# Kernel optimization log

Measured on AMD Instinct MI355X. Metric: run time of the kernel, lower is better.

Reference implementation:

```python
import math
import jax, jax.numpy as jnp
import numpy as np
from jax.scipy.special import xlogy, gammaln

DIM = 768
HEADS = 8
DIM_KEY = 64
DIM_VALUE = 64
NUM_REL_POS_FEATURES = 192
B = 2
N = 2048


def get_positional_embed(seq_len, feature_size):
    # distances: [-n+1, ..., n-1], length 2n-1
    dist = jnp.arange(-seq_len + 1, seq_len).astype(jnp.float32)
    ad = jnp.abs(dist)[:, None]  # [2n-1, 1]
    nb = feature_size // 6  # num basis per class (3 fns, doubled by sign concat)

    # exponential
    max_range = math.log(seq_len) / math.log(2.0)
    half_life = 2.0 ** jnp.linspace(3.0, max_range, nb)  # min_half_life = 3.0
    f_exp = jnp.exp(-math.log(2.0) / half_life[None, :] * ad)

    # central mask
    widths = 2.0 ** jnp.arange(1, nb + 1).astype(jnp.float32) - 1.0
    f_cm = (widths[None, :] > ad).astype(jnp.float32)

    # gamma pdf
    stddev = seq_len / (2.0 * nb)
    start_mean = seq_len / nb
    mean = jnp.linspace(start_mean, float(seq_len), nb)[None, :]
    conc = (mean / stddev) ** 2
    rate = mean / (stddev ** 2)
    log_unnorm = xlogy(conc - 1.0, ad) - rate * ad
    log_norm = gammaln(conc) - conc * jnp.log(rate)
    prob = jnp.exp(log_unnorm - log_norm) + 1e-8
    f_g = prob / jnp.max(prob, axis=-1, keepdims=True)

    emb = jnp.concatenate([f_exp, f_cm, f_g], axis=-1)  # [2n-1, 3*nb]
    emb = jnp.concatenate([emb, jnp.sign(dist)[:, None] * emb], axis=-1)  # [2n-1, 6*nb]
    return emb


def relative_shift(x):
    # x: [b, h, t1, 2*t1 - 1] -> [b, h, t1, t1] via pad/reshape trick
    b, h, t1, t2 = x.shape
    x = jnp.pad(x, ((0, 0), (0, 0), (0, 0), (1, 0)))  # [b,h,t1,t2+1]
    x = x.reshape(b, h, t2 + 1, t1)[:, :, 1:, :].reshape(b, h, t1, t2)
    return x[..., : (t2 + 2) // 2]


def setup_inputs() -> dict:
    key = jax.random.key(0)
    ks = jax.random.split(key, 9)
    dk, dv, h = DIM_KEY, DIM_VALUE, HEADS
    s_in = 1.0 / math.sqrt(DIM)
    s_rel = 1.0 / math.sqrt(NUM_REL_POS_FEATURES)
    s_out = 1.0 / math.sqrt(dv * h)
    return {
        "x": jax.random.normal(ks[0], (B, N, DIM), dtype=jnp.float32),
        # weights stored [in, out] (torch Linear weight transposed)
        "Wq": jax.random.normal(ks[1], (DIM, dk * h), dtype=jnp.float32) * s_in,
        "Wk": jax.random.normal(ks[2], (DIM, dk * h), dtype=jnp.float32) * s_in,
        "Wv": jax.random.normal(ks[3], (DIM, dv * h), dtype=jnp.float32) * s_in,
        "Wrel": jax.random.normal(ks[4], (NUM_REL_POS_FEATURES, dk * h), dtype=jnp.float32) * s_rel,
        # module inits to_out at zeros; use random values for a meaningful baseline
        "Wout": jax.random.normal(ks[5], (dv * h, DIM), dtype=jnp.float32) * s_out,
        "b_out": jax.random.normal(ks[6], (DIM,), dtype=jnp.float32) * 0.01,
        "rel_content_bias": jax.random.normal(ks[7], (1, h, 1, dk), dtype=jnp.float32),
        "rel_pos_bias": jax.random.normal(ks[8], (1, h, 1, dk), dtype=jnp.float32),
    }


def reference(x, Wq, Wk, Wv, Wrel, Wout, b_out, rel_content_bias, rel_pos_bias):
    b, n, _ = x.shape
    h, dk = HEADS, DIM_KEY
    scale = dk ** -0.5

    q = (x @ Wq).reshape(b, n, h, dk).transpose(0, 2, 1, 3) * scale  # [b,h,n,dk]
    k = (x @ Wk).reshape(b, n, h, dk).transpose(0, 2, 1, 3)
    v = (x @ Wv).reshape(b, n, h, -1).transpose(0, 2, 1, 3)  # [b,h,n,dv]

    content_logits = jnp.einsum('bhid,bhjd->bhij', q + rel_content_bias, k)

    positions = get_positional_embed(n, NUM_REL_POS_FEATURES)  # [2n-1, F]
    rel_k = (positions @ Wrel).reshape(2 * n - 1, h, dk).transpose(1, 0, 2)  # [h,2n-1,dk]
    rel_logits = jnp.einsum('bhid,hjd->bhij', q + rel_pos_bias, rel_k)  # [b,h,n,2n-1]
    rel_logits = relative_shift(rel_logits)  # [b,h,n,n]

    attn = jax.nn.softmax(content_logits + rel_logits, axis=-1)
    out = jnp.einsum('bhij,bhjd->bhid', attn, v)  # [b,h,n,dv]
    out = out.transpose(0, 2, 1, 3).reshape(b, n, -1)  # [b,n,h*dv]
    return out @ Wout + b_out
```

## Files before the change

### kernel.cpp

```cpp
#include <hip/hip_runtime.h>
#include <hip/hip_bf16.h>
#include <math.h>
#include <stdint.h>

typedef __hip_bfloat16 bf16;
typedef __attribute__((ext_vector_type(8))) short short8;
typedef __attribute__((ext_vector_type(4))) float f32x4;

#define SEQ   2048
#define NPOS  4095
#define DIMM  768
#define HEADS 8
#define DK    64
#define HD    512
#define BATCH 2
#define BH    16
#define ROWS  4096

#define OB_RELK  ((size_t)0)
#define OB_QC    ((size_t)4194304)
#define OB_QP    ((size_t)8388608)
#define OB_K     ((size_t)12582912)
#define OB_V     ((size_t)16777216)
#define OB_OH    ((size_t)20971520)
#define OB_EMBH  OB_OH
#define OB_EMBL  ((size_t)(OB_OH + 1572864))
#define OB_VT    OB_OH
#define OB_XH    ((size_t)25165824)
#define OB_XL    ((size_t)31457280)
#define OB_WQKVH ((size_t)37748736)
#define OB_WQKVL ((size_t)40108032)
#define OB_OP    ((size_t)25165824)
#define OB_LP    ((size_t)41943040)
#define OB_WOH   ((size_t)42467328)
#define OB_WOL   ((size_t)43253760)
#define OB_WRH   ((size_t)44040192)
#define OB_WRL   ((size_t)44236800)

__device__ __forceinline__ unsigned f2bf(float f) {
  unsigned u = __float_as_uint(f);
  return (u + 0x7fffu + ((u >> 16) & 1u)) >> 16;
}
__device__ __forceinline__ void split2(float v, unsigned& hb, unsigned& lb) {
  hb = f2bf(v);
  const float back = __uint_as_float(hb << 16);
  lb = f2bf(v - back);
}

__device__ __forceinline__ void cp16(const short* g, short* l) {
  __builtin_amdgcn_global_load_lds(
      (__attribute__((address_space(1))) void*)(uintptr_t)(g),
      (__attribute__((address_space(3))) void*)(uint32_t)(uintptr_t)(l),
      16, 0, 0);
}

__global__ __launch_bounds__(256) void prep_all(
    const float* __restrict__ x,
    const float* __restrict__ Wq, const float* __restrict__ Wk,
    const float* __restrict__ Wv, const float* __restrict__ Wout,
    const float* __restrict__ Wrel,
    short* __restrict__ eh, short* __restrict__ el,
    short* __restrict__ xh, short* __restrict__ xl,
    short* __restrict__ wqkvh, short* __restrict__ wqkvl,
    short* __restrict__ woh, short* __restrict__ wol,
    short* __restrict__ wrh, short* __restrict__ wrl) {
  __shared__ float tile[32][33];
  const int blk = blockIdx.x;
  const int t = threadIdx.x;

  if (blk < 512) {
    const int row = blk * 8 + (t >> 5);
    const int j   = t & 31;
    if (row >= NPOS) {
      for (int c = j; c < 192; c += 32) { eh[(size_t)row * 192 + c] = 0; el[(size_t)row * 192 + c] = 0; }
      return;
    }
    const float dist = (float)(row - (SEQ - 1));
    const float ad   = fabsf(dist);
    const float hl    = exp2f(3.0f + 8.0f * (float)j / 31.0f);
    const float f_exp = exp2f(-ad / hl);
    const float width = exp2f((float)(j + 1)) - 1.0f;
    const float f_cm  = (width > ad) ? 1.0f : 0.0f;
    float prob;
    if (ad > 0.0f) {
      const float c   = 4.0f * (float)((j + 1) * (j + 1));
      const float r   = (float)(j + 1) / 16.0f;
      const float lu  = (c - 1.0f) * logf(ad) - r * ad;
      const float ln_ = lgammaf(c) - c * logf(r);
      prob = expf(lu - ln_) + 1e-8f;
    } else {
      prob = 1e-8f;
    }
    float mx = prob;
    for (int off = 16; off; off >>= 1) mx = fmaxf(mx, __shfl_xor(mx, off, 32));
    const float f_g = prob / mx;
    const float s = (dist > 0.f) ? 1.f : ((dist < 0.f) ? -1.f : 0.f);
    const float vals[6] = {f_exp, f_cm, f_g, s * f_exp, s * f_cm, s * f_g};
    short* ph = eh + (size_t)row * 192;
    short* pl = el + (size_t)row * 192;
#pragma unroll
    for (int q = 0; q < 6; q++) {
      unsigned hb, lb;
      split2(vals[q], hb, lb);
      ph[q * 32 + j] = (short)hb;
      pl[q * 32 + j] = (short)lb;
    }
    return;
  }

  if (blk < 3584) {
    const int i = (blk - 512) * 256 + t;
    const float4 v = ((const float4*)x)[i];
    unsigned h0, l0, h1, l1, h2, l2, h3, l3;
    split2(v.x, h0, l0); split2(v.y, h1, l1); split2(v.z, h2, l2); split2(v.w, h3, l3);
    *(uint2*)&xh[(size_t)i * 4] = make_uint2(h0 | (h1 << 16), h2 | (h3 << 16));
    *(uint2*)&xl[(size_t)i * 4] = make_uint2(l0 | (l1 << 16), l2 | (l3 << 16));
    return;
  }

  const float* src; short* dh; short* dl; int R, C, local;
  if (blk < 3968)      { local = blk - 3584; src = Wq;   dh = wqkvh;               dl = wqkvl;               R = DIMM; C = HD; }
  else if (blk < 4352) { local = blk - 3968; src = Wk;   dh = wqkvh + 512 * DIMM;  dl = wqkvl + 512 * DIMM;  R = DIMM; C = HD; }
  else if (blk < 4736) { local = blk - 4352; src = Wv;   dh = wqkvh + 1024 * DIMM; dl = wqkvl + 1024 * DIMM; R = DIMM; C = HD; }
  else if (blk < 5120) { local = blk - 4736; src = Wout; dh = woh;  dl = wol;  R = HD;  C = DIMM; }
  else                 { local = blk - 5120; src = Wrel; dh = wrh;  dl = wrl;  R = 192; C = HD; }
  const int ctiles = C / 32;
  const int c0 = (local % ctiles) * 32, r0 = (local / ctiles) * 32;
  {
    const int lr = t >> 3, lc = (t & 7) * 4;
    const float4 v = *(const float4*)&src[(size_t)(r0 + lr) * C + c0 + lc];
    tile[lr][lc] = v.x; tile[lr][lc + 1] = v.y; tile[lr][lc + 2] = v.z; tile[lr][lc + 3] = v.w;
  }
  __syncthreads();
  const int nn = t >> 3, kb = (t & 7) * 4;
  unsigned hb[4], lb[4];
#pragma unroll
  for (int e = 0; e < 4; e++) split2(tile[kb + e][nn], hb[e], lb[e]);
  const size_t o = (size_t)(c0 + nn) * R + r0 + kb;
  *(uint2*)&dh[o] = make_uint2(hb[0] | (hb[1] << 16), hb[2] | (hb[3] << 16));
  *(uint2*)&dl[o] = make_uint2(lb[0] | (lb[1] << 16), lb[2] | (lb[3] << 16));
}

__global__ void vtrans_kernel(const short* __restrict__ vv, short* __restrict__ vt) {
  __shared__ short tile[64][72];
  const int t = threadIdx.x;
  const int s0 = blockIdx.x * 64, bh = blockIdx.y;
  {
    const int sl = t >> 2, dc = (t & 3) * 16;
    const short* src = vv + ((size_t)bh * SEQ + s0 + sl) * DK + dc;
    *(uint4*)&tile[sl][dc]     = *(const uint4*)src;
    *(uint4*)&tile[sl][dc + 8] = *(const uint4*)(src + 8);
  }
  __syncthreads();
  const int dr = t >> 6, sc = t & 63;
#pragma unroll
  for (int it = 0; it < 16; it++) {
    const int d = it * 4 + dr;
    vt[((size_t)bh * DK + d) * SEQ + s0 + sc] = tile[sc][d];
  }
}

__global__ __launch_bounds__(256) void gemm_qr(
    const short* __restrict__ xh, const short* __restrict__ xl,
    const short* __restrict__ wqkvh, const short* __restrict__ wqkvl,
    const short* __restrict__ eh, const short* __restrict__ el,
    const short* __restrict__ wrh, const short* __restrict__ wrl,
    const float* __restrict__ cb, const float* __restrict__ pb,
    bf16* __restrict__ oq, bf16* __restrict__ oqp,
    bf16* __restrict__ ok, bf16* __restrict__ ov,
    bf16* __restrict__ relk) {
  __shared__ short AsH[128][32];
  __shared__ short AsL[128][32];
  __shared__ short BsH[128][32];
  __shared__ short BsL[128][32];

  const int bx = blockIdx.x;
  const bool isq = bx < 384;
  const int lbx = isq ? bx : bx - 384;
  const int mt = lbx & 31, ntile = lbx >> 5;
  const int m0 = mt * 128, n0 = ntile * 128;
  const int KD = isq ? DIMM : 192;
  const short* Ah = isq ? xh : eh;
  const short* Al = isq ? xl : el;
  const short* Bh = isq ? wqkvh : wrh;
  const short* Bl = isq ? wqkvl : wrl;

  const int t = threadIdx.x, lane = t & 63, w = t >> 6;
  const int quad = lane >> 4, l15 = lane & 15;
  const int wm = (w >> 1) * 64, wn = (w & 1) * 64;

  const int srow = w * 32 + (lane >> 2);
  const int skof = (lane & 3) * 8;

  f32x4 acc[4][4];
#pragma unroll
  for (int i = 0; i < 4; i++)
#pragma unroll
    for (int j = 0; j < 4; j++) acc[i][j] = (f32x4){0.f, 0.f, 0.f, 0.f};

  for (int k0 = 0; k0 < KD; k0 += 32) {
    __syncthreads();
#pragma unroll
    for (int c = 0; c < 2; c++) {
      const size_t ra = (size_t)(m0 + srow + c * 16) * KD + k0 + skof;
      const size_t rb = (size_t)(n0 + srow + c * 16) * KD + k0 + skof;
      short* la = &AsH[w * 32 + c * 16][0];
      cp16(&Ah[ra], la);
      cp16(&Al[ra], &AsL[w * 32 + c * 16][0]);
      cp16(&Bh[rb], &BsH[w * 32 + c * 16][0]);
      cp16(&Bl[rb], &BsL[w * 32 + c * 16][0]);
    }
    __syncthreads();

    short8 amh[4], aml[4], bnh[4], bnl[4];
#pragma unroll
    for (int i = 0; i < 4; i++) {
      amh[i] = *(const short8*)&AsH[wm + i * 16 + l15][quad * 8];
      aml[i] = *(const short8*)&AsL[wm + i * 16 + l15][quad * 8];
      bnh[i] = *(const short8*)&BsH[wn + i * 16 + l15][quad * 8];
      bnl[i] = *(const short8*)&BsL[wn + i * 16 + l15][quad * 8];
    }
#pragma unroll
    for (int i = 0; i < 4; i++) {
#pragma unroll
      for (int j = 0; j < 4; j++) {
        acc[i][j] = __builtin_amdgcn_mfma_f32_16x16x32_bf16(amh[i], bnh[j], acc[i][j], 0, 0, 0);
        acc[i][j] = __builtin_amdgcn_mfma_f32_16x16x32_bf16(amh[i], bnl[j], acc[i][j], 0, 0, 0);
        acc[i][j] = __builtin_amdgcn_mfma_f32_16x16x32_bf16(aml[i], bnh[j], acc[i][j], 0, 0, 0);
      }
    }
  }

  if (isq) {
    const int sel = ntile >> 2;
#pragma unroll
    for (int i = 0; i < 4; i++) {
#pragma unroll
      for (int j = 0; j < 4; j++) {
        const int n = n0 + wn + j * 16 + l15;
        const int hd_ = n & 511, hh = hd_ >> 6, d = hd_ & 63;
#pragma unroll
        for (int g = 0; g < 4; g++) {
          const int m = m0 + wm + i * 16 + quad * 4 + g;
          const int b = m >> 11, s = m & 2047;
          const size_t idx = (((size_t)(b * HEADS + hh) * SEQ) + s) * DK + d;
          const float v = acc[i][j][g];
          if (sel == 0) {
            const float sv = v * 0.125f;
            oq[idx]  = __float2bfloat16(sv + cb[hh * DK + d]);
            oqp[idx] = __float2bfloat16(sv + pb[hh * DK + d]);
          } else if (sel == 1) {
            ok[idx] = __float2bfloat16(v);
          } else {
            ov[idx] = __float2bfloat16(v);
          }
        }
      }
    }
  } else {
#pragma unroll
    for (int i = 0; i < 4; i++) {
#pragma unroll
      for (int j = 0; j < 4; j++) {
        const int n = n0 + wn + j * 16 + l15;
        const int hh = n >> 6, d = n & 63;
#pragma unroll
        for (int g = 0; g < 4; g++) {
          const int m = m0 + wm + i * 16 + quad * 4 + g;
          if (m < NPOS) relk[((size_t)hh * NPOS + m) * DK + d] = __float2bfloat16(acc[i][j][g]);
        }
      }
    }
  }
}

__global__ __launch_bounds__(256) void out_gemm(
    const short* __restrict__ Ahp,
    const short* __restrict__ Bhp, const short* __restrict__ Blp,
    const float* __restrict__ bias, float* __restrict__ ofp) {
  __shared__ short AsH[128][32];
  __shared__ short BsH[128][32];
  __shared__ short BsL[128][32];

  const int t = threadIdx.x, lane = t & 63, w = t >> 6;
  const int quad = lane >> 4, l15 = lane & 15;
  const int wm = (w >> 1) * 64, wn = (w & 1) * 64;
  const int m0 = blockIdx.x * 128, n0 = blockIdx.y * 128;
  const int srow = w * 32 + (lane >> 2);
  const int skof = (lane & 3) * 8;

  f32x4 acc[4][4];
#pragma unroll
  for (int i = 0; i < 4; i++)
#pragma unroll
    for (int j = 0; j < 4; j++) acc[i][j] = (f32x4){0.f, 0.f, 0.f, 0.f};

  for (int k0 = 0; k0 < HD; k0 += 32) {
    __syncthreads();
#pragma unroll
    for (int c = 0; c < 2; c++) {
      const size_t ra = (size_t)(m0 + srow + c * 16) * HD + k0 + skof;
      const size_t rb = (size_t)(n0 + srow + c * 16) * HD + k0 + skof;
      cp16(&Ahp[ra], &AsH[w * 32 + c * 16][0]);
      cp16(&Bhp[rb], &BsH[w * 32 + c * 16][0]);
      cp16(&Blp[rb], &BsL[w * 32 + c * 16][0]);
    }
    __syncthreads();

    short8 amh[4], bnh[4], bnl[4];
#pragma unroll
    for (int i = 0; i < 4; i++) {
      amh[i] = *(const short8*)&AsH[wm + i * 16 + l15][quad * 8];
      bnh[i] = *(const short8*)&BsH[wn + i * 16 + l15][quad * 8];
      bnl[i] = *(const short8*)&BsL[wn + i * 16 + l15][quad * 8];
    }
#pragma unroll
    for (int i = 0; i < 4; i++) {
#pragma unroll
      for (int j = 0; j < 4; j++) {
        acc[i][j] = __builtin_amdgcn_mfma_f32_16x16x32_bf16(amh[i], bnh[j], acc[i][j], 0, 0, 0);
        acc[i][j] = __builtin_amdgcn_mfma_f32_16x16x32_bf16(amh[i], bnl[j], acc[i][j], 0, 0, 0);
      }
    }
  }

#pragma unroll
  for (int i = 0; i < 4; i++) {
#pragma unroll
    for (int j = 0; j < 4; j++) {
      const int n = n0 + wn + j * 16 + l15;
      const float bv = bias[n];
#pragma unroll
      for (int g = 0; g < 4; g++) {
        const int m = m0 + wm + i * 16 + quad * 4 + g;
        ofp[(size_t)m * DIMM + n] = acc[i][j][g] + bv;
      }
    }
  }
}

__global__ __launch_bounds__(256) void attn_mfma4(
    const short* __restrict__ qc, const short* __restrict__ qp,
    const short* __restrict__ kg, const short* __restrict__ vt,
    const short* __restrict__ relk,
    float* __restrict__ Op, float* __restrict__ Lp) {
  __shared__ short Rel_lds[128][72];
  __shared__ short Vt_lds[64][72];
  __shared__ short Pw[4][16][72];

  const int t    = threadIdx.x;
  const int lane = t & 63;
  const int w    = t >> 6;
  const int quad = lane >> 4;
  const int l15  = lane & 15;
  const int bh   = blockIdx.y;
  const int h    = bh & 7;
  const int i0   = blockIdx.x * 64;
  const int z    = blockIdx.z;
  const int jb   = z * (SEQ / 2);

  short8 qcA[2], qpA[2];
  {
    const size_t qrow = ((size_t)bh * SEQ + i0 + w * 16 + l15) * DK + quad * 8;
    qcA[0] = *(const short8*)(qc + qrow);
    qcA[1] = *(const short8*)(qc + qrow + 32);
    qpA[0] = *(const short8*)(qp + qrow);
    qpA[1] = *(const short8*)(qp + qrow + 32);
  }

  int idxg[4]; bool selg[4];
#pragma unroll
  for (int g = 0; g < 4; g++) {
    const int r = quad * 4 + g;
    idxg[g] = (((lane & 48) | ((l15 + 15 - r) & 15)) << 2);
    selg[g] = (l15 <= r);
  }

  short8 ones8;
#pragma unroll
  for (int e = 0; e < 8; e++) ones8[e] = (short)0x3F80;

  f32x4 oacc[4];
#pragma unroll
  for (int dt = 0; dt < 4; dt++) oacc[dt] = (f32x4){0.f, 0.f, 0.f, 0.f};
  f32x4 lacc = (f32x4){0.f, 0.f, 0.f, 0.f};

  const short* kbase = kg + (size_t)bh * SEQ * DK;
  const short* vbase = vt + (size_t)bh * DK * SEQ;
  const short* rbase = relk + (size_t)h * NPOS * DK;

  const int rr  = t >> 1, rcc = (t & 1) * 32;
  const int vr  = t >> 2, vcc = (t & 3) * 16;
  const int rb_w = 48 - 16 * w;

  for (int jt = 0; jt < SEQ / 2 / 64; jt++) {
    const int j0 = jb + jt * 64;

    __syncthreads();
    {
      const short* src = rbase + (size_t)((j0 - i0 + 1984) + rr) * DK + rcc;
      *(uint4*)&Rel_lds[rr][rcc]      = *(const uint4*)(src);
      *(uint4*)&Rel_lds[rr][rcc + 8]  = *(const uint4*)(src + 8);
      *(uint4*)&Rel_lds[rr][rcc + 16] = *(const uint4*)(src + 16);
      *(uint4*)&Rel_lds[rr][rcc + 24] = *(const uint4*)(src + 24);
    }
    {
      const short* src = vbase + (size_t)vr * SEQ + j0 + vcc;
      *(uint4*)&Vt_lds[vr][vcc]     = *(const uint4*)(src);
      *(uint4*)&Vt_lds[vr][vcc + 8] = *(const uint4*)(src + 8);
    }
    __syncthreads();

    f32x4 sacc[4];
#pragma unroll
    for (int nt = 0; nt < 4; nt++) {
      const short* kr = kbase + (size_t)(j0 + nt * 16 + l15) * DK + quad * 8;
      short8 b0 = *(const short8*)kr;
      short8 b1 = *(const short8*)(kr + 32);
      f32x4 a = (f32x4){0.f, 0.f, 0.f, 0.f};
      a = __builtin_amdgcn_mfma_f32_16x16x32_bf16(qcA[0], b0, a, 0, 0, 0);
      a = __builtin_amdgcn_mfma_f32_16x16x32_bf16(qcA[1], b1, a, 0, 0, 0);
      sacc[nt] = a;
    }

    f32x4 rprev;
    {
      const short* rl = &Rel_lds[rb_w + l15][quad * 8];
      short8 b0 = *(const short8*)rl;
      short8 b1 = *(const short8*)(rl + 32);
      f32x4 a = (f32x4){0.f, 0.f, 0.f, 0.f};
      a = __builtin_amdgcn_mfma_f32_16x16x32_bf16(qpA[0], b0, a, 0, 0, 0);
      a = __builtin_amdgcn_mfma_f32_16x16x32_bf16(qpA[1], b1, a, 0, 0, 0);
      rprev = a;
    }
    f32x4 bpp;
#pragma unroll
    for (int g = 0; g < 4; g++)
      bpp[g] = __int_as_float(__builtin_amdgcn_ds_bpermute(idxg[g], __float_as_int(rprev[g])));

#pragma unroll
    for (int nt = 0; nt < 4; nt++) {
      f32x4 rcur;
      {
        const short* rl = &Rel_lds[rb_w + (nt + 1) * 16 + l15][quad * 8];
        short8 b0 = *(const short8*)rl;
        short8 b1 = *(const short8*)(rl + 32);
        f32x4 a = (f32x4){0.f, 0.f, 0.f, 0.f};
        a = __builtin_amdgcn_mfma_f32_16x16x32_bf16(qpA[0], b0, a, 0, 0, 0);
        a = __builtin_amdgcn_mfma_f32_16x16x32_bf16(qpA[1], b1, a, 0, 0, 0);
        rcur = a;
      }
      f32x4 bpc;
#pragma unroll
      for (int g = 0; g < 4; g++)
        bpc[g] = __int_as_float(__builtin_amdgcn_ds_bpermute(idxg[g], __float_as_int(rcur[g])));
#pragma unroll
      for (int g = 0; g < 4; g++) {
        const float relv = selg[g] ? bpp[g] : bpc[g];
        const float s = sacc[nt][g] + relv;
        const float p = __expf(s - 12.0f);
        Pw[w][quad * 4 + g][nt * 16 + l15] = (short)f2bf(p);
      }
      bpp = bpc;
    }

#pragma unroll
    for (int ks = 0; ks < 2; ks++) {
      short8 pA = *(const short8*)&Pw[w][l15][ks * 32 + quad * 8];
      lacc = __builtin_amdgcn_mfma_f32_16x16x32_bf16(pA, ones8, lacc, 0, 0, 0);
#pragma unroll
      for (int dt = 0; dt < 4; dt++) {
        short8 vB = *(const short8*)&Vt_lds[dt * 16 + l15][ks * 32 + quad * 8];
        oacc[dt] = __builtin_amdgcn_mfma_f32_16x16x32_bf16(pA, vB, oacc[dt], 0, 0, 0);
      }
    }
  }

  const size_t obase = ((size_t)(z * BH + bh) * SEQ + i0 + w * 16);
#pragma unroll
  for (int g = 0; g < 4; g++) {
    const int r = quad * 4 + g;
#pragma unroll
    for (int dt = 0; dt < 4; dt++)
      Op[(obase + r) * DK + dt * 16 + l15] = oacc[dt][g];
    if (l15 == 0) Lp[obase + r] = lacc[g];
  }
}

__global__ void merge_kernel(const float* __restrict__ Op, const float* __restrict__ Lp,
                             bf16* __restrict__ oh) {
  const int gid = blockIdx.x * 256 + threadIdx.x;
  const int m = gid >> 7;
  const int n0 = (gid & 127) * 4;
  const int b = m >> 11, s = m & 2047;
  const int hh = n0 >> 6, d0 = n0 & 63;
  const int bh = b * HEADS + hh;
  const float l = Lp[(size_t)bh * SEQ + s] + Lp[((size_t)BH + bh) * SEQ + s];
  const float inv = 1.0f / l;
  const float4 o0 = *(const float4*)&Op[((size_t)bh * SEQ + s) * DK + d0];
  const float4 o1 = *(const float4*)&Op[(((size_t)BH + bh) * SEQ + s) * DK + d0];
  *(uint2*)&oh[(size_t)m * HD + n0] = make_uint2(
      f2bf((o0.x + o1.x) * inv) | (f2bf((o0.y + o1.y) * inv) << 16),
      f2bf((o0.z + o1.z) * inv) | (f2bf((o0.w + o1.w) * inv) << 16));
}

extern "C" void kernel_launch(void* const* d_in, const int* in_sizes, int n_in,
                              void* d_out, int out_size, void* d_ws, size_t ws_size,
                              hipStream_t stream) {
  (void)in_sizes; (void)n_in; (void)out_size; (void)ws_size;
  const float* x    = (const float*)d_in[0];
  const float* Wq   = (const float*)d_in[1];
  const float* Wk   = (const float*)d_in[2];
  const float* Wv   = (const float*)d_in[3];
  const float* Wrel = (const float*)d_in[4];
  const float* Wout = (const float*)d_in[5];
  const float* bout = (const float*)d_in[6];
  const float* cb   = (const float*)d_in[7];
  const float* pb   = (const float*)d_in[8];
  float* out = (float*)d_out;

  char* ws = (char*)d_ws;
  bf16*  relk = (bf16*)(ws + OB_RELK);
  bf16*  qc   = (bf16*)(ws + OB_QC);
  bf16*  qp   = (bf16*)(ws + OB_QP);
  bf16*  kk   = (bf16*)(ws + OB_K);
  bf16*  vv   = (bf16*)(ws + OB_V);
  bf16*  oh   = (bf16*)(ws + OB_OH);
  short* vt   = (short*)(ws + OB_VT);
  float* Opb  = (float*)(ws + OB_OP);
  float* Lpb  = (float*)(ws + OB_LP);
  short* embh = (short*)(ws + OB_EMBH);
  short* embl = (short*)(ws + OB_EMBL);
  short* xh   = (short*)(ws + OB_XH);
  short* xl   = (short*)(ws + OB_XL);
  short* wqh  = (short*)(ws + OB_WQKVH);
  short* wql  = (short*)(ws + OB_WQKVL);
  short* woh  = (short*)(ws + OB_WOH);
  short* wol  = (short*)(ws + OB_WOL);
  short* wrh  = (short*)(ws + OB_WRH);
  short* wrl  = (short*)(ws + OB_WRL);

  hipLaunchKernelGGL(prep_all, dim3(5216), dim3(256), 0, stream,
                     x, Wq, Wk, Wv, Wout, Wrel,
                     embh, embl, xh, xl, wqh, wql, woh, wol, wrh, wrl);
  hipLaunchKernelGGL(gemm_qr, dim3(512), dim3(256), 0, stream,
                     xh, xl, wqh, wql, embh, embl, wrh, wrl,
                     cb, pb, qc, qp, kk, vv, relk);
  hipLaunchKernelGGL(vtrans_kernel, dim3(SEQ / 64, BH), dim3(256), 0, stream,
                     (const short*)vv, vt);
  hipLaunchKernelGGL(attn_mfma4, dim3(SEQ / 64, BH, 2), dim3(256), 0, stream,
                     (const short*)qc, (const short*)qp, (const short*)kk,
                     (const short*)vt, (const short*)relk, Opb, Lpb);
  hipLaunchKernelGGL(merge_kernel, dim3(ROWS * (HD / 4) / 256), dim3(256), 0, stream,
                     Opb, Lpb, oh);
  hipLaunchKernelGGL(out_gemm, dim3(32, 6), dim3(256), 0, stream,
                     (const short*)oh, woh, wol, bout, out);
}
```

Before: 246.1 us.

## Read rel-pos keys and V directly from global memory, drop LDS staging

Removes the shared-memory staging of rel_k and V tiles, along with the two block-wide barriers per iteration, and reads MFMA B operands straight from global memory. The rel-pos projection for the first 16 columns is computed once before the loop, and the last tile's permuted result is carried into the next iteration, so each iteration does four rel-pos tiles instead of five. Each wave now issues its own global loads, relying on L1/L2 for reuse across waves, and the strided V-transpose reads and row reads of rel_k may be less coalesced.

```diff
diff --git a/kernel.cpp b/kernel.cpp
--- a/kernel.cpp
+++ b/kernel.cpp
@@ -344,8 +344,6 @@
     const short* __restrict__ kg, const short* __restrict__ vt,
     const short* __restrict__ relk,
     float* __restrict__ Op, float* __restrict__ Lp) {
-  __shared__ short Rel_lds[128][72];
-  __shared__ short Vt_lds[64][72];
   __shared__ short Pw[4][16][72];
 
   const int t    = threadIdx.x;
@@ -387,29 +385,25 @@
 
   const short* kbase = kg + (size_t)bh * SEQ * DK;
   const short* vbase = vt + (size_t)bh * DK * SEQ;
-  const short* rbase = relk + (size_t)h * NPOS * DK;
-
-  const int rr  = t >> 1, rcc = (t & 1) * 32;
-  const int vr  = t >> 2, vcc = (t & 3) * 16;
+  const short* rbase = relk + ((size_t)h * NPOS + (size_t)(1984 - i0)) * DK;
+
   const int rb_w = 48 - 16 * w;
+
+  f32x4 bpp_carry;
+  {
+    const short* rl = rbase + (size_t)(jb + rb_w + l15) * DK + quad * 8;
+    short8 b0 = *(const short8*)rl;
+    short8 b1 = *(const short8*)(rl + 32);
+    f32x4 a = (f32x4){0.f, 0.f, 0.f, 0.f};
+    a = __builtin_amdgcn_mfma_f32_16x16x32_bf16(qpA[0], b0, a, 0, 0, 0);
+    a = __builtin_amdgcn_mfma_f32_16x16x32_bf16(qpA[1], b1, a, 0, 0, 0);
+#pragma unroll
+    for (int g = 0; g < 4; g++)
+      bpp_carry[g] = __int_as_float(__builtin_amdgcn_ds_bpermute(idxg[g], __float_as_int(a[g])));
+  }
 
   for (int jt = 0; jt < SEQ / 2 / 64; jt++) {
     const int j0 = jb + jt * 64;
-
-    __syncthreads();
-    {
-      const short* src = rbase + (size_t)((j0 - i0 + 1984) + rr) * DK + rcc;
-      *(uint4*)&Rel_lds[rr][rcc]      = *(const uint4*)(src);
-      *(uint4*)&Rel_lds[rr][rcc + 8]  = *(const uint4*)(src + 8);
-      *(uint4*)&Rel_lds[rr][rcc + 16] = *(const uint4*)(src + 16);
-      *(uint4*)&Rel_lds[rr][rcc + 24] = *(const uint4*)(src + 24);
-    }
-    {
-      const short* src = vbase + (size_t)vr * SEQ + j0 + vcc;
-      *(uint4*)&Vt_lds[vr][vcc]     = *(const uint4*)(src);
-      *(uint4*)&Vt_lds[vr][vcc + 8] = *(const uint4*)(src + 8);
-    }
-    __syncthreads();
 
     f32x4 sacc[4];
 #pragma unroll
@@ -423,26 +417,13 @@
       sacc[nt] = a;
     }
 
-    f32x4 rprev;
-    {
-      const short* rl = &Rel_lds[rb_w + l15][quad * 8];
-      short8 b0 = *(const short8*)rl;
-      short8 b1 = *(const short8*)(rl + 32);
-      f32x4 a = (f32x4){0.f, 0.f, 0.f, 0.f};
-      a = __builtin_amdgcn_mfma_f32_16x16x32_bf16(qpA[0], b0, a, 0, 0, 0);
-      a = __builtin_amdgcn_mfma_f32_16x16x32_bf16(qpA[1], b1, a, 0, 0, 0);
-      rprev = a;
-    }
-    f32x4 bpp;
-#pragma unroll
-    for (int g = 0; g < 4; g++)
-      bpp[g] = __int_as_float(__builtin_amdgcn_ds_bpermute(idxg[g], __float_as_int(rprev[g])));
+    f32x4 bpp = bpp_carry;
 
 #pragma unroll
     for (int nt = 0; nt < 4; nt++) {
       f32x4 rcur;
       {
-        const short* rl = &Rel_lds[rb_w + (nt + 1) * 16 + l15][quad * 8];
+        const short* rl = rbase + (size_t)(j0 + rb_w + (nt + 1) * 16 + l15) * DK + quad * 8;
         short8 b0 = *(const short8*)rl;
         short8 b1 = *(const short8*)(rl + 32);
         f32x4 a = (f32x4){0.f, 0.f, 0.f, 0.f};
@@ -463,6 +444,7 @@
       }
       bpp = bpc;
     }
+    bpp_carry = bpp;
 
 #pragma unroll
     for (int ks = 0; ks < 2; ks++) {
@@ -470,7 +452,8 @@
       lacc = __builtin_amdgcn_mfma_f32_16x16x32_bf16(pA, ones8, lacc, 0, 0, 0);
 #pragma unroll
       for (int dt = 0; dt < 4; dt++) {
-        short8 vB = *(const short8*)&Vt_lds[dt * 16 + l15][ks * 32 + quad * 8];
+        const short* vr = vbase + (size_t)(dt * 16 + l15) * SEQ + j0 + ks * 32 + quad * 8;
+        short8 vB = *(const short8*)vr;
         oacc[dt] = __builtin_amdgcn_mfma_f32_16x16x32_bf16(pA, vB, oacc[dt], 0, 0, 0);
       }
     }
```

New measurement: 326.9 us. +32.8%, slower.

## Fuse V transpose into QKV GEMM epilogue, carry rel-logit tile, swizzle attention grid

Applied to the files above, without the earlier changes.

The separate V-transpose kernel is removed. The QKV GEMM epilogue now writes V directly in transposed [bh][d][seq] layout as packed 4-element bf16 stores. In the attention kernel, the relative-logit tile for the previous block is carried across iterations in registers instead of being recomputed each tile, so fewer rel rows are loaded into LDS. The grid is also flattened to 1D with a block swizzle, which changes how blocks map onto CUs and caches. The risks are strided uint2 stores in the GEMM epilogue and a more complex index mapping.

```diff
diff --git a/kernel.cpp b/kernel.cpp
--- a/kernel.cpp
+++ b/kernel.cpp
@@ -25,7 +25,6 @@
 #define OB_OH    ((size_t)20971520)
 #define OB_EMBH  OB_OH
 #define OB_EMBL  ((size_t)(OB_OH + 1572864))
-#define OB_VT    OB_OH
 #define OB_XH    ((size_t)25165824)
 #define OB_XL    ((size_t)31457280)
 #define OB_WQKVH ((size_t)37748736)
@@ -141,25 +140,6 @@
   *(uint2*)&dl[o] = make_uint2(lb[0] | (lb[1] << 16), lb[2] | (lb[3] << 16));
 }
 
-__global__ void vtrans_kernel(const short* __restrict__ vv, short* __restrict__ vt) {
-  __shared__ short tile[64][72];
-  const int t = threadIdx.x;
-  const int s0 = blockIdx.x * 64, bh = blockIdx.y;
-  {
-    const int sl = t >> 2, dc = (t & 3) * 16;
-    const short* src = vv + ((size_t)bh * SEQ + s0 + sl) * DK + dc;
-    *(uint4*)&tile[sl][dc]     = *(const uint4*)src;
-    *(uint4*)&tile[sl][dc + 8] = *(const uint4*)(src + 8);
-  }
-  __syncthreads();
-  const int dr = t >> 6, sc = t & 63;
-#pragma unroll
-  for (int it = 0; it < 16; it++) {
-    const int d = it * 4 + dr;
-    vt[((size_t)bh * DK + d) * SEQ + s0 + sc] = tile[sc][d];
-  }
-}
-
 __global__ __launch_bounds__(256) void gemm_qr(
     const short* __restrict__ xh, const short* __restrict__ xl,
     const short* __restrict__ wqkvh, const short* __restrict__ wqkvl,
@@ -167,7 +147,7 @@
     const short* __restrict__ wrh, const short* __restrict__ wrl,
     const float* __restrict__ cb, const float* __restrict__ pb,
     bf16* __restrict__ oq, bf16* __restrict__ oqp,
-    bf16* __restrict__ ok, bf16* __restrict__ ov,
+    bf16* __restrict__ ok, short* __restrict__ vtw,
     bf16* __restrict__ relk) {
   __shared__ short AsH[128][32];
   __shared__ short AsL[128][32];
@@ -204,8 +184,7 @@
     for (int c = 0; c < 2; c++) {
       const size_t ra = (size_t)(m0 + srow + c * 16) * KD + k0 + skof;
       const size_t rb = (size_t)(n0 + srow + c * 16) * KD + k0 + skof;
-      short* la = &AsH[w * 32 + c * 16][0];
-      cp16(&Ah[ra], la);
+      cp16(&Ah[ra], &AsH[w * 32 + c * 16][0]);
       cp16(&Al[ra], &AsL[w * 32 + c * 16][0]);
       cp16(&Bh[rb], &BsH[w * 32 + c * 16][0]);
       cp16(&Bl[rb], &BsL[w * 32 + c * 16][0]);
@@ -233,26 +212,41 @@
 
   if (isq) {
     const int sel = ntile >> 2;
-#pragma unroll
-    for (int i = 0; i < 4; i++) {
-#pragma unroll
-      for (int j = 0; j < 4; j++) {
-        const int n = n0 + wn + j * 16 + l15;
-        const int hd_ = n & 511, hh = hd_ >> 6, d = hd_ & 63;
-#pragma unroll
-        for (int g = 0; g < 4; g++) {
-          const int m = m0 + wm + i * 16 + quad * 4 + g;
+    if (sel == 2) {
+#pragma unroll
+      for (int i = 0; i < 4; i++) {
+#pragma unroll
+        for (int j = 0; j < 4; j++) {
+          const int n = n0 + wn + j * 16 + l15;
+          const int hd_ = n & 511, hh = hd_ >> 6, d = hd_ & 63;
+          const int m = m0 + wm + i * 16 + quad * 4;
           const int b = m >> 11, s = m & 2047;
-          const size_t idx = (((size_t)(b * HEADS + hh) * SEQ) + s) * DK + d;
-          const float v = acc[i][j][g];
-          if (sel == 0) {
-            const float sv = v * 0.125f;
-            oq[idx]  = __float2bfloat16(sv + cb[hh * DK + d]);
-            oqp[idx] = __float2bfloat16(sv + pb[hh * DK + d]);
-          } else if (sel == 1) {
-            ok[idx] = __float2bfloat16(v);
-          } else {
-            ov[idx] = __float2bfloat16(v);
+          const uint2 pk = make_uint2(
+              f2bf(acc[i][j][0]) | (f2bf(acc[i][j][1]) << 16),
+              f2bf(acc[i][j][2]) | (f2bf(acc[i][j][3]) << 16));
+          *(uint2*)&vtw[(((size_t)(b * HEADS + hh) * DK + d) * SEQ) + s] = pk;
+        }
+      }
+    } else {
+#pragma unroll
+      for (int i = 0; i < 4; i++) {
+#pragma unroll
+        for (int j = 0; j < 4; j++) {
+          const int n = n0 + wn + j * 16 + l15;
+          const int hd_ = n & 511, hh = hd_ >> 6, d = hd_ & 63;
+#pragma unroll
+          for (int g = 0; g < 4; g++) {
+            const int m = m0 + wm + i * 16 + quad * 4 + g;
+            const int b = m >> 11, s = m & 2047;
+            const size_t idx = (((size_t)(b * HEADS + hh) * SEQ) + s) * DK + d;
+            const float v = acc[i][j][g];
+            if (sel == 0) {
+              const float sv = v * 0.125f;
+              oq[idx]  = __float2bfloat16(sv + cb[hh * DK + d]);
+              oqp[idx] = __float2bfloat16(sv + pb[hh * DK + d]);
+            } else {
+              ok[idx] = __float2bfloat16(v);
+            }
           }
         }
       }
@@ -348,16 +342,19 @@
   __shared__ short Vt_lds[64][72];
   __shared__ short Pw[4][16][72];
 
+  const int bid = blockIdx.x;
+  const int swz = (bid & 7) * 128 + (bid >> 3);
+  const int i0  = (swz & 31) * 64;
+  const int bh  = (swz >> 5) & 15;
+  const int z   = swz >> 9;
+  const int h   = bh & 7;
+  const int jb  = z * (SEQ / 2);
+
   const int t    = threadIdx.x;
   const int lane = t & 63;
   const int w    = t >> 6;
   const int quad = lane >> 4;
   const int l15  = lane & 15;
-  const int bh   = blockIdx.y;
-  const int h    = bh & 7;
-  const int i0   = blockIdx.x * 64;
-  const int z    = blockIdx.z;
-  const int jb   = z * (SEQ / 2);
 
   short8 qcA[2], qpA[2];
   {
@@ -387,18 +384,31 @@
 
   const short* kbase = kg + (size_t)bh * SEQ * DK;
   const short* vbase = vt + (size_t)bh * DK * SEQ;
-  const short* rbase = relk + (size_t)h * NPOS * DK;
-
-  const int rr  = t >> 1, rcc = (t & 1) * 32;
+  const short* rbase = relk + ((size_t)(h * NPOS + 1984 - i0)) * DK;
+
+  const int rr  = 16 + (t >> 1), rcc = (t & 1) * 32;
   const int vr  = t >> 2, vcc = (t & 3) * 16;
   const int rb_w = 48 - 16 * w;
 
+  f32x4 bpp_carry;
+  {
+    const short* rl = rbase + (size_t)(jb + rb_w + l15) * DK + quad * 8;
+    short8 b0 = *(const short8*)rl;
+    short8 b1 = *(const short8*)(rl + 32);
+    f32x4 a = (f32x4){0.f, 0.f, 0.f, 0.f};
+    a = __builtin_amdgcn_mfma_f32_16x16x32_bf16(qpA[0], b0, a, 0, 0, 0);
+    a = __builtin_amdgcn_mfma_f32_16x16x32_bf16(qpA[1], b1, a, 0, 0, 0);
+#pragma unroll
+    for (int g = 0; g < 4; g++)
+      bpp_carry[g] = __int_as_float(__builtin_amdgcn_ds_bpermute(idxg[g], __float_as_int(a[g])));
+  }
+
   for (int jt = 0; jt < SEQ / 2 / 64; jt++) {
     const int j0 = jb + jt * 64;
 
     __syncthreads();
-    {
-      const short* src = rbase + (size_t)((j0 - i0 + 1984) + rr) * DK + rcc;
+    if (rr < 128) {
+      const short* src = rbase + (size_t)(j0 + rr) * DK + rcc;
       *(uint4*)&Rel_lds[rr][rcc]      = *(const uint4*)(src);
       *(uint4*)&Rel_lds[rr][rcc + 8]  = *(const uint4*)(src + 8);
       *(uint4*)&Rel_lds[rr][rcc + 16] = *(const uint4*)(src + 16);
@@ -423,20 +433,7 @@
       sacc[nt] = a;
     }
 
-    f32x4 rprev;
-    {
-      const short* rl = &Rel_lds[rb_w + l15][quad * 8];
-      short8 b0 = *(const short8*)rl;
-      short8 b1 = *(const short8*)(rl + 32);
-      f32x4 a = (f32x4){0.f, 0.f, 0.f, 0.f};
-      a = __builtin_amdgcn_mfma_f32_16x16x32_bf16(qpA[0], b0, a, 0, 0, 0);
-      a = __builtin_amdgcn_mfma_f32_16x16x32_bf16(qpA[1], b1, a, 0, 0, 0);
-      rprev = a;
-    }
-    f32x4 bpp;
-#pragma unroll
-    for (int g = 0; g < 4; g++)
-      bpp[g] = __int_as_float(__builtin_amdgcn_ds_bpermute(idxg[g], __float_as_int(rprev[g])));
+    f32x4 bpp = bpp_carry;
 
 #pragma unroll
     for (int nt = 0; nt < 4; nt++) {
@@ -463,6 +460,7 @@
       }
       bpp = bpc;
     }
+    bpp_carry = bpp;
 
 #pragma unroll
     for (int ks = 0; ks < 2; ks++) {
@@ -524,9 +522,8 @@
   bf16*  qc   = (bf16*)(ws + OB_QC);
   bf16*  qp   = (bf16*)(ws + OB_QP);
   bf16*  kk   = (bf16*)(ws + OB_K);
-  bf16*  vv   = (bf16*)(ws + OB_V);
+  short* vt   = (short*)(ws + OB_V);
   bf16*  oh   = (bf16*)(ws + OB_OH);
-  short* vt   = (short*)(ws + OB_VT);
   float* Opb  = (float*)(ws + OB_OP);
   float* Lpb  = (float*)(ws + OB_LP);
   short* embh = (short*)(ws + OB_EMBH);
@@ -545,10 +542,8 @@
                      embh, embl, xh, xl, wqh, wql, woh, wol, wrh, wrl);
   hipLaunchKernelGGL(gemm_qr, dim3(512), dim3(256), 0, stream,
                      xh, xl, wqh, wql, embh, embl, wrh, wrl,
-                     cb, pb, qc, qp, kk, vv, relk);
-  hipLaunchKernelGGL(vtrans_kernel, dim3(SEQ / 64, BH), dim3(256), 0, stream,
-                     (const short*)vv, vt);
-  hipLaunchKernelGGL(attn_mfma4, dim3(SEQ / 64, BH, 2), dim3(256), 0, stream,
+                     cb, pb, qc, qp, kk, vt, relk);
+  hipLaunchKernelGGL(attn_mfma4, dim3(1024), dim3(256), 0, stream,
                      (const short*)qc, (const short*)qp, (const short*)kk,
                      (const short*)vt, (const short*)relk, Opb, Lpb);
   hipLaunchKernelGGL(merge_kernel, dim3(ROWS * (HD / 4) / 256), dim3(256), 0, stream,
```

Result: faster. 236.3 us (-4.0%).
